# Optimization experiments

Hardware: AMD Instinct MI355X
Metric: run time of the kernel (lower is better)

The kernel has to match this reference:

```python
import jax, jax.numpy as jnp
import numpy as np

N_NODES = 50000
N_EDGES = 800000
D_IN = 64
D_HID = 64
D_OUT = 64


def setup_inputs() -> dict:
    key = jax.random.key(0)
    ks = jax.random.split(key, 9)
    x = jax.random.normal(ks[0], (N_NODES, D_IN), dtype=jnp.float32)
    src = jax.random.randint(ks[1], (N_EDGES,), 0, N_NODES, dtype=jnp.int64)
    dst = jax.random.randint(ks[2], (N_EDGES,), 0, N_NODES, dtype=jnp.int64)
    s0 = 1.0 / np.sqrt(D_IN)
    s1 = 1.0 / np.sqrt(D_HID)
    W_self0 = jax.random.normal(ks[3], (D_IN, D_HID), dtype=jnp.float32) * s0
    W_neigh0 = jax.random.normal(ks[4], (D_IN, D_HID), dtype=jnp.float32) * s0
    b0 = jnp.zeros((D_HID,), dtype=jnp.float32)
    W_self1 = jax.random.normal(ks[5], (D_HID, D_OUT), dtype=jnp.float32) * s1
    W_neigh1 = jax.random.normal(ks[6], (D_HID, D_OUT), dtype=jnp.float32) * s1
    b1 = jnp.zeros((D_OUT,), dtype=jnp.float32)
    return {"x": x, "src": src, "dst": dst,
            "W_self0": W_self0, "W_neigh0": W_neigh0, "b0": b0,
            "W_self1": W_self1, "W_neigh1": W_neigh1, "b1": b1}


def reference(x, src, dst, W_self0, W_neigh0, b0, W_self1, W_neigh1, b1):
    n = x.shape[0]
    # in-degree per destination node; clamp to 1 for isolated nodes (DGL behavior)
    deg = jax.ops.segment_sum(jnp.ones(src.shape[0], dtype=x.dtype), dst, num_segments=n)
    inv_deg = (1.0 / jnp.maximum(deg, 1.0))[:, None]  # [N,1]

    def sage_mean(h, W_self, W_neigh, b):
        # gather src features, mean-reduce onto dst, then linear combine
        agg = jax.ops.segment_sum(h[src], dst, num_segments=n)  # [N,d]
        neigh = agg * inv_deg
        return h @ W_self + neigh @ W_neigh + b

    # layer 0: SAGEConv with internal relu activation
    h = jax.nn.relu(sage_mean(x, W_self0, W_neigh0, b0))
    # outer relu in GraphSAGE_Full.forward (idempotent after internal relu)
    h = jax.nn.relu(h)
    # dropout rate 0.0 -> identity
    # final layer: no activation
    h = sage_mean(h, W_self1, W_neigh1, b1)
    return h
```

## Files before the change

### kernel.cpp

```cpp
#include <hip/hip_runtime.h>

#define N_NODES 50000
#define N_EDGES 800000
#define D 64
#define NSLICE 8
#define SLICE_N ((N_NODES + NSLICE - 1) / NSLICE)
#define BCAP 64

__device__ __forceinline__ unsigned short f2bf(float f) {
    unsigned int u = __builtin_bit_cast(unsigned int, f);
    u += 0x7fffu + ((u >> 16) & 1u);
    return (unsigned short)(u >> 16);
}
__device__ __forceinline__ float bflo(unsigned int u) {
    return __builtin_bit_cast(float, u << 16);
}
__device__ __forceinline__ float bfhi(unsigned int u) {
    return __builtin_bit_cast(float, u & 0xffff0000u);
}

__global__ __launch_bounds__(256) void k_fill2(const int* __restrict__ src,
                                               const int* __restrict__ dst,
                                               int* __restrict__ cnt,
                                               int* __restrict__ csr) {
    int slice = blockIdx.x & (NSLICE - 1);
    int lo = slice * SLICE_N, hi = lo + SLICE_N;
    int gblk = blockIdx.x >> 3, nblk = gridDim.x >> 3;
    for (int e = gblk * blockDim.x + threadIdx.x; e < N_EDGES; e += nblk * blockDim.x) {
        int d = dst[e];
        if (d >= lo && d < hi) {
            int p = atomicAdd(&cnt[d], 1);
            csr[(d << 6) + p] = src[e];
        }
    }
}

__global__ __launch_bounds__(256, 4) void k_xform(const float* __restrict__ h,
        const float* __restrict__ Ws, const float* __restrict__ Wn,
        const float* __restrict__ b,
        float* __restrict__ yS, unsigned short* __restrict__ yN,
        int* __restrict__ cnt, int zero_cnt) {
    if (zero_cnt && blockIdx.x < 196) {
        int i = blockIdx.x * 256 + threadIdx.x;
        if (i < N_NODES) cnt[i] = 0;
    }
    int lane = threadIdx.x & 63;
    int gwave = __builtin_amdgcn_readfirstlane((blockIdx.x * blockDim.x + threadIdx.x) >> 6);
    int nwaves = (gridDim.x * blockDim.x) >> 6;

    int mat = gwave & 1;
    const float* W = mat ? Wn : Ws;

    float w[D];
#pragma unroll
    for (int k = 0; k < D; ++k) w[k] = W[k * D + lane];
    float bj = mat ? 0.f : b[lane];

    const int ngroups = (N_NODES + 3) / 4;
    for (int g = gwave >> 1; g < ngroups; g += (nwaves >> 1)) {
        const float* x0 = h + (size_t)(g * 4) * D;
        float a0 = bj, a1 = bj, a2 = bj, a3 = bj;
#pragma unroll
        for (int kq = 0; kq < 16; ++kq) {
            float4 v0 = *(const float4*)(x0 + 0 * D + kq * 4);
            float4 v1 = *(const float4*)(x0 + 1 * D + kq * 4);
            float4 v2 = *(const float4*)(x0 + 2 * D + kq * 4);
            float4 v3 = *(const float4*)(x0 + 3 * D + kq * 4);
            a0 = fmaf(v0.x, w[kq * 4 + 0], a0);
            a1 = fmaf(v1.x, w[kq * 4 + 0], a1);
            a2 = fmaf(v2.x, w[kq * 4 + 0], a2);
            a3 = fmaf(v3.x, w[kq * 4 + 0], a3);
            a0 = fmaf(v0.y, w[kq * 4 + 1], a0);
            a1 = fmaf(v1.y, w[kq * 4 + 1], a1);
            a2 = fmaf(v2.y, w[kq * 4 + 1], a2);
            a3 = fmaf(v3.y, w[kq * 4 + 1], a3);
            a0 = fmaf(v0.z, w[kq * 4 + 2], a0);
            a1 = fmaf(v1.z, w[kq * 4 + 2], a1);
            a2 = fmaf(v2.z, w[kq * 4 + 2], a2);
            a3 = fmaf(v3.z, w[kq * 4 + 2], a3);
            a0 = fmaf(v0.w, w[kq * 4 + 3], a0);
            a1 = fmaf(v1.w, w[kq * 4 + 3], a1);
            a2 = fmaf(v2.w, w[kq * 4 + 3], a2);
            a3 = fmaf(v3.w, w[kq * 4 + 3], a3);
        }
        size_t base = (size_t)(g * 4) * D + lane;
        if (mat) {
            yN[base + 0 * D] = f2bf(a0);
            yN[base + 1 * D] = f2bf(a1);
            yN[base + 2 * D] = f2bf(a2);
            yN[base + 3 * D] = f2bf(a3);
        } else {
            yS[base + 0 * D] = a0;
            yS[base + 1 * D] = a1;
            yS[base + 2 * D] = a2;
            yS[base + 3 * D] = a3;
        }
    }
}

__global__ __launch_bounds__(256) void k_aggf(const char* __restrict__ yN,
        const float* __restrict__ yS,
        const int* __restrict__ cnt, const int* __restrict__ csr,
        float* __restrict__ out, int relu) {
    int node = __builtin_amdgcn_readfirstlane((blockIdx.x * blockDim.x + threadIdx.x) >> 6);
    int lane = threadIdx.x & 63;
    int q = lane >> 3;
    int fq = lane & 7;
    int deg = cnt[node];
    const int* bucket = csr + (node << 6);
    unsigned foff = (unsigned)fq * 16u;

    float s0 = 0.f, s1 = 0.f, s2 = 0.f, s3 = 0.f;
    float s4 = 0.f, s5 = 0.f, s6 = 0.f, s7 = 0.f;

#define ROUND16(E0)                                                         \
    {                                                                       \
        int i0 = (E0) + q, i1 = i0 + 8;                                     \
        int b0 = bucket[i0], b1 = bucket[i1];                               \
        unsigned a0 = (i0 < deg) ? ((unsigned)b0 << 7) : 0u;                \
        unsigned a1 = (i1 < deg) ? ((unsigned)b1 << 7) : 0u;                \
        float m0 = (i0 < deg) ? 1.f : 0.f;                                  \
        float m1 = (i1 < deg) ? 1.f : 0.f;                                  \
        uint4 u0 = *(const uint4*)(yN + a0 + foff);                         \
        uint4 u1 = *(const uint4*)(yN + a1 + foff);                         \
        s0 = fmaf(m0, bflo(u0.x), s0); s0 = fmaf(m1, bflo(u1.x), s0);       \
        s1 = fmaf(m0, bfhi(u0.x), s1); s1 = fmaf(m1, bfhi(u1.x), s1);       \
        s2 = fmaf(m0, bflo(u0.y), s2); s2 = fmaf(m1, bflo(u1.y), s2);       \
        s3 = fmaf(m0, bfhi(u0.y), s3); s3 = fmaf(m1, bfhi(u1.y), s3);       \
        s4 = fmaf(m0, bflo(u0.z), s4); s4 = fmaf(m1, bflo(u1.z), s4);       \
        s5 = fmaf(m0, bfhi(u0.z), s5); s5 = fmaf(m1, bfhi(u1.z), s5);       \
        s6 = fmaf(m0, bflo(u0.w), s6); s6 = fmaf(m1, bflo(u1.w), s6);       \
        s7 = fmaf(m0, bfhi(u0.w), s7); s7 = fmaf(m1, bfhi(u1.w), s7);       \
    }

    ROUND16(0)
    if (deg > 16) ROUND16(16)
    if (deg > 32) {
        ROUND16(32)
        if (deg > 48) ROUND16(48)
    }
#undef ROUND16

    s0 += __shfl_xor(s0, 8, 64); s0 += __shfl_xor(s0, 16, 64); s0 += __shfl_xor(s0, 32, 64);
    s1 += __shfl_xor(s1, 8, 64); s1 += __shfl_xor(s1, 16, 64); s1 += __shfl_xor(s1, 32, 64);
    s2 += __shfl_xor(s2, 8, 64); s2 += __shfl_xor(s2, 16, 64); s2 += __shfl_xor(s2, 32, 64);
    s3 += __shfl_xor(s3, 8, 64); s3 += __shfl_xor(s3, 16, 64); s3 += __shfl_xor(s3, 32, 64);
    s4 += __shfl_xor(s4, 8, 64); s4 += __shfl_xor(s4, 16, 64); s4 += __shfl_xor(s4, 32, 64);
    s5 += __shfl_xor(s5, 8, 64); s5 += __shfl_xor(s5, 16, 64); s5 += __shfl_xor(s5, 32, 64);
    s6 += __shfl_xor(s6, 8, 64); s6 += __shfl_xor(s6, 16, 64); s6 += __shfl_xor(s6, 32, 64);
    s7 += __shfl_xor(s7, 8, 64); s7 += __shfl_xor(s7, 16, 64); s7 += __shfl_xor(s7, 32, 64);

    float sv = (q == 0) ? s0 : (q == 1) ? s1 : (q == 2) ? s2 : (q == 3) ? s3
             : (q == 4) ? s4 : (q == 5) ? s5 : (q == 6) ? s6 : s7;
    int f = fq * 8 + q;
    float self = yS[(size_t)node * D + f];
    float inv = 1.0f / fmaxf((float)deg, 1.0f);
    float acc = self + sv * inv;
    if (relu) acc = fmaxf(acc, 0.f);
    out[(size_t)node * D + f] = acc;
}

extern "C" void kernel_launch(void* const* d_in, const int* in_sizes, int n_in,
                              void* d_out, int out_size, void* d_ws, size_t ws_size,
                              hipStream_t stream) {
    const float* x   = (const float*)d_in[0];
    const int*   src = (const int*)d_in[1];
    const int*   dst = (const int*)d_in[2];
    const float* Ws0 = (const float*)d_in[3];
    const float* Wn0 = (const float*)d_in[4];
    const float* b0  = (const float*)d_in[5];
    const float* Ws1 = (const float*)d_in[6];
    const float* Wn1 = (const float*)d_in[7];
    const float* b1  = (const float*)d_in[8];
    float* out = (float*)d_out;

    char* p = (char*)d_ws;
    float*          yS  = (float*)p;          p += (size_t)N_NODES * D * sizeof(float);
    unsigned short* yN  = (unsigned short*)p; p += (size_t)N_NODES * D * sizeof(unsigned short);
    int* cnt = (int*)p;                       p += (size_t)N_NODES * sizeof(int);
    int* csr = (int*)p;                       p += (size_t)N_NODES * BCAP * sizeof(int);

    const int aggBlocks = (N_NODES + 3) / 4;

    k_xform<<<1024, 256, 0, stream>>>(x, Ws0, Wn0, b0, yS, yN, cnt, 1);
    k_fill2<<<1024, 256, 0, stream>>>(src, dst, cnt, csr);
    k_aggf<<<aggBlocks, 256, 0, stream>>>((const char*)yN, yS, cnt, csr, out, 1);

    k_xform<<<1024, 256, 0, stream>>>(out, Ws1, Wn1, b1, yS, yN, cnt, 0);
    k_aggf<<<aggBlocks, 256, 0, stream>>>((const char*)yN, yS, cnt, csr, out, 0);
}
```

Before: 197.5 us.

## Fuse layer-0 aggregation with layer-1 linear transform into one kernel

Layer-0 neighbor aggregation now feeds straight into the layer-1 self and neighbor matmuls inside a new kernel. Each wave aggregates 8 nodes, stages each hidden row in shared memory, and multiplies it by both weight matrices held in registers. This removes the round trip of the hidden activations through global memory and one kernel launch. In exchange each thread holds 128 weight registers, which may lower occupancy, and each wave handles nodes one after another with less gather parallelism.

Result: slower. 228.7 us (+15.8%).

```diff
diff --git a/kernel.cpp b/kernel.cpp
--- a/kernel.cpp
+++ b/kernel.cpp
@@ -98,14 +98,9 @@
     }
 }
 
-__global__ __launch_bounds__(256) void k_aggf(const char* __restrict__ yN,
-        const float* __restrict__ yS,
-        const int* __restrict__ cnt, const int* __restrict__ csr,
-        float* __restrict__ out, int relu) {
-    int node = __builtin_amdgcn_readfirstlane((blockIdx.x * blockDim.x + threadIdx.x) >> 6);
-    int lane = threadIdx.x & 63;
-    int q = lane >> 3;
-    int fq = lane & 7;
+__device__ __forceinline__ float gather_h(const char* __restrict__ yN,
+        const float* __restrict__ yS, const int* __restrict__ cnt,
+        const int* __restrict__ csr, int node, int q, int fq, int relu) {
     int deg = cnt[node];
     const int* bucket = csr + (node << 6);
     unsigned foff = (unsigned)fq * 16u;
@@ -157,7 +152,70 @@
     float inv = 1.0f / fmaxf((float)deg, 1.0f);
     float acc = self + sv * inv;
     if (relu) acc = fmaxf(acc, 0.f);
-    out[(size_t)node * D + f] = acc;
+    return acc;
+}
+
+__global__ __launch_bounds__(256) void k_aggx(const char* __restrict__ yN,
+        const float* __restrict__ yS,
+        const int* __restrict__ cnt, const int* __restrict__ csr,
+        const float* __restrict__ Ws1, const float* __restrict__ Wn1,
+        const float* __restrict__ b1,
+        float* __restrict__ yS2, unsigned short* __restrict__ yN2) {
+    __shared__ float hrow[4][D];
+    int lane = threadIdx.x & 63;
+    int wib  = threadIdx.x >> 6;
+    int gwave = __builtin_amdgcn_readfirstlane(blockIdx.x * 4 + wib);
+    int q = lane >> 3;
+    int fq = lane & 7;
+    int f = fq * 8 + q;
+
+    float wsc[D], wnc[D];
+#pragma unroll
+    for (int k = 0; k < D; ++k) {
+        wsc[k] = Ws1[k * D + lane];
+        wnc[k] = Wn1[k * D + lane];
+    }
+    float bj = b1[lane];
+    float* myrow = hrow[wib];
+
+    int node0 = gwave * 8;
+#pragma unroll 1
+    for (int it = 0; it < 8; ++it) {
+        int node = node0 + it;
+        if (node >= N_NODES) break;
+
+        float h = gather_h(yN, yS, cnt, csr, node, q, fq, 1);
+        myrow[f] = h;
+
+        float a0 = bj, a1 = 0.f;
+#pragma unroll
+        for (int kq = 0; kq < 16; ++kq) {
+            float4 hk = *(const float4*)(&myrow[kq * 4]);
+            a0 = fmaf(hk.x, wsc[kq * 4 + 0], a0);
+            a1 = fmaf(hk.x, wnc[kq * 4 + 0], a1);
+            a0 = fmaf(hk.y, wsc[kq * 4 + 1], a0);
+            a1 = fmaf(hk.y, wnc[kq * 4 + 1], a1);
+            a0 = fmaf(hk.z, wsc[kq * 4 + 2], a0);
+            a1 = fmaf(hk.z, wnc[kq * 4 + 2], a1);
+            a0 = fmaf(hk.w, wsc[kq * 4 + 3], a0);
+            a1 = fmaf(hk.w, wnc[kq * 4 + 3], a1);
+        }
+        size_t base = (size_t)node * D + lane;
+        yS2[base] = a0;
+        yN2[base] = f2bf(a1);
+    }
+}
+
+__global__ __launch_bounds__(256) void k_aggf(const char* __restrict__ yN,
+        const float* __restrict__ yS,
+        const int* __restrict__ cnt, const int* __restrict__ csr,
+        float* __restrict__ out, int relu) {
+    int node = __builtin_amdgcn_readfirstlane((blockIdx.x * blockDim.x + threadIdx.x) >> 6);
+    int lane = threadIdx.x & 63;
+    int q = lane >> 3;
+    int fq = lane & 7;
+    float acc = gather_h(yN, yS, cnt, csr, node, q, fq, relu);
+    out[(size_t)node * D + fq * 8 + q] = acc;
 }
 
 extern "C" void kernel_launch(void* const* d_in, const int* in_sizes, int n_in,
@@ -177,15 +235,17 @@
     char* p = (char*)d_ws;
     float*          yS  = (float*)p;          p += (size_t)N_NODES * D * sizeof(float);
     unsigned short* yN  = (unsigned short*)p; p += (size_t)N_NODES * D * sizeof(unsigned short);
+    float*          yS2 = (float*)p;          p += (size_t)N_NODES * D * sizeof(float);
+    unsigned short* yN2 = (unsigned short*)p; p += (size_t)N_NODES * D * sizeof(unsigned short);
     int* cnt = (int*)p;                       p += (size_t)N_NODES * sizeof(int);
     int* csr = (int*)p;                       p += (size_t)N_NODES * BCAP * sizeof(int);
 
-    const int aggBlocks = (N_NODES + 3) / 4;
+    const int aggBlocks  = (N_NODES + 3) / 4;
+    const int aggxBlocks = (N_NODES + 31) / 32;
 
     k_xform<<<1024, 256, 0, stream>>>(x, Ws0, Wn0, b0, yS, yN, cnt, 1);
     k_fill2<<<1024, 256, 0, stream>>>(src, dst, cnt, csr);
-    k_aggf<<<aggBlocks, 256, 0, stream>>>((const char*)yN, yS, cnt, csr, out, 1);
-
-    k_xform<<<1024, 256, 0, stream>>>(out, Ws1, Wn1, b1, yS, yN, cnt, 0);
-    k_aggf<<<aggBlocks, 256, 0, stream>>>((const char*)yN, yS, cnt, csr, out, 0);
-}
+    k_aggx<<<aggxBlocks, 256, 0, stream>>>((const char*)yN, yS, cnt, csr,
+                                           Ws1, Wn1, b1, yS2, yN2);
+    k_aggf<<<aggBlocks, 256, 0, stream>>>((const char*)yN2, yS2, cnt, csr, out, 0);
+}
```

## Merge layer-0 transform and CSR fill into one role-split kernel

Applied to the files above, without the earlier changes.

Fuses the first-layer feature transform and the edge bucketing into a single launch where even blocks run the transform and odd blocks fill the CSR buckets, so the two independent stages can overlap on the GPU. The counter zeroing moves out of the transform kernel into a hipMemsetAsync. This removes a kernel boundary and lets the compute-bound transform run alongside the atomic-heavy fill. The cost is an extra memset launch, and the fused kernel loses the occupancy hint of 4 blocks per SM in its launch bounds.

After: 189.5 us. 4.0% less time.

```diff
diff --git a/kernel.cpp b/kernel.cpp
--- a/kernel.cpp
+++ b/kernel.cpp
@@ -19,35 +19,11 @@
     return __builtin_bit_cast(float, u & 0xffff0000u);
 }
 
-__global__ __launch_bounds__(256) void k_fill2(const int* __restrict__ src,
-                                               const int* __restrict__ dst,
-                                               int* __restrict__ cnt,
-                                               int* __restrict__ csr) {
-    int slice = blockIdx.x & (NSLICE - 1);
-    int lo = slice * SLICE_N, hi = lo + SLICE_N;
-    int gblk = blockIdx.x >> 3, nblk = gridDim.x >> 3;
-    for (int e = gblk * blockDim.x + threadIdx.x; e < N_EDGES; e += nblk * blockDim.x) {
-        int d = dst[e];
-        if (d >= lo && d < hi) {
-            int p = atomicAdd(&cnt[d], 1);
-            csr[(d << 6) + p] = src[e];
-        }
-    }
-}
-
-__global__ __launch_bounds__(256, 4) void k_xform(const float* __restrict__ h,
+__device__ __forceinline__ void xform_body(const float* __restrict__ h,
         const float* __restrict__ Ws, const float* __restrict__ Wn,
         const float* __restrict__ b,
         float* __restrict__ yS, unsigned short* __restrict__ yN,
-        int* __restrict__ cnt, int zero_cnt) {
-    if (zero_cnt && blockIdx.x < 196) {
-        int i = blockIdx.x * 256 + threadIdx.x;
-        if (i < N_NODES) cnt[i] = 0;
-    }
-    int lane = threadIdx.x & 63;
-    int gwave = __builtin_amdgcn_readfirstlane((blockIdx.x * blockDim.x + threadIdx.x) >> 6);
-    int nwaves = (gridDim.x * blockDim.x) >> 6;
-
+        int gwave, int nwaves, int lane) {
     int mat = gwave & 1;
     const float* W = mat ? Wn : Ws;
 
@@ -98,6 +74,42 @@
     }
 }
 
+__global__ __launch_bounds__(256) void k_pre(const float* __restrict__ x,
+        const float* __restrict__ Ws0, const float* __restrict__ Wn0,
+        const float* __restrict__ b0,
+        float* __restrict__ yS, unsigned short* __restrict__ yN,
+        const int* __restrict__ src, const int* __restrict__ dst,
+        int* __restrict__ cnt, int* __restrict__ csr) {
+    int role = blockIdx.x & 1;
+    int sub  = blockIdx.x >> 1;
+    if (role == 0) {
+        int lane = threadIdx.x & 63;
+        int gwave = __builtin_amdgcn_readfirstlane(sub * 4 + (int)(threadIdx.x >> 6));
+        xform_body(x, Ws0, Wn0, b0, yS, yN, gwave, 4096, lane);
+    } else {
+        int slice = sub & (NSLICE - 1);
+        int lo = slice * SLICE_N, hi = lo + SLICE_N;
+        int gblk = sub >> 3, nblk = 1024 >> 3;
+        for (int e = gblk * 256 + (int)threadIdx.x; e < N_EDGES; e += nblk * 256) {
+            int d = dst[e];
+            if (d >= lo && d < hi) {
+                int p = atomicAdd(&cnt[d], 1);
+                csr[(d << 6) + p] = src[e];
+            }
+        }
+    }
+}
+
+__global__ __launch_bounds__(256, 4) void k_xform(const float* __restrict__ h,
+        const float* __restrict__ Ws, const float* __restrict__ Wn,
+        const float* __restrict__ b,
+        float* __restrict__ yS, unsigned short* __restrict__ yN) {
+    int lane = threadIdx.x & 63;
+    int gwave = __builtin_amdgcn_readfirstlane((blockIdx.x * blockDim.x + threadIdx.x) >> 6);
+    int nwaves = (gridDim.x * blockDim.x) >> 6;
+    xform_body(h, Ws, Wn, b, yS, yN, gwave, nwaves, lane);
+}
+
 __global__ __launch_bounds__(256) void k_aggf(const char* __restrict__ yN,
         const float* __restrict__ yS,
         const int* __restrict__ cnt, const int* __restrict__ csr,
@@ -182,10 +194,12 @@
 
     const int aggBlocks = (N_NODES + 3) / 4;
 
-    k_xform<<<1024, 256, 0, stream>>>(x, Ws0, Wn0, b0, yS, yN, cnt, 1);
-    k_fill2<<<1024, 256, 0, stream>>>(src, dst, cnt, csr);
+    hipMemsetAsync(cnt, 0, (size_t)N_NODES * sizeof(int), stream);
+
+    k_pre<<<2048, 256, 0, stream>>>(x, Ws0, Wn0, b0, yS, yN, src, dst, cnt, csr);
+
     k_aggf<<<aggBlocks, 256, 0, stream>>>((const char*)yN, yS, cnt, csr, out, 1);
 
-    k_xform<<<1024, 256, 0, stream>>>(out, Ws1, Wn1, b1, yS, yN, cnt, 0);
+    k_xform<<<1024, 256, 0, stream>>>(out, Ws1, Wn1, b1, yS, yN);
     k_aggf<<<aggBlocks, 256, 0, stream>>>((const char*)yN, yS, cnt, csr, out, 0);
 }
```
